# Kernel optimization log

Hardware: AMD Instinct MI355X
Metric: run time of the kernel (lower is better)

The kernel has to match this reference:

```python
import jax, jax.numpy as jnp
import numpy as np

B, S, D, H, DEPTH, VOCAB = 4096, 64, 512, 8, 4, 2
HD = D // H
EPS = 1e-5


def setup_inputs() -> dict:
    key = jax.random.key(0)
    ks = jax.random.split(key, 12)
    sc = 0.02
    return {
        "a_seq": jax.random.randint(ks[0], (B, S), 0, VOCAB, dtype=jnp.int32),
        "b_seq": jax.random.randint(ks[1], (B, S), 0, VOCAB, dtype=jnp.int32),
        "bit_emb": jax.random.normal(ks[2], (VOCAB, D), jnp.float32),
        "start_state": jax.random.normal(ks[3], (D,), jnp.float32),
        "ln1_g": jnp.ones((DEPTH, D), jnp.float32),
        "ln1_b": jnp.zeros((DEPTH, D), jnp.float32),
        # weights stored [in, out] (transpose of torch nn.Linear layout)
        "qkv_w": jax.random.normal(ks[4], (DEPTH, D, 3 * D), jnp.float32) * sc,
        "qkv_b": jnp.zeros((DEPTH, 3 * D), jnp.float32),
        "out_w": jax.random.normal(ks[5], (DEPTH, D, D), jnp.float32) * sc,
        "out_b": jnp.zeros((DEPTH, D), jnp.float32),
        "ln2_g": jnp.ones((DEPTH, D), jnp.float32),
        "ln2_b": jnp.zeros((DEPTH, D), jnp.float32),
        "ff1_w": jax.random.normal(ks[6], (DEPTH, D, 4 * D), jnp.float32) * sc,
        "ff1_b": jnp.zeros((DEPTH, 4 * D), jnp.float32),
        "ff2_w": jax.random.normal(ks[7], (DEPTH, 4 * D, D), jnp.float32) * sc,
        "ff2_b": jnp.zeros((DEPTH, D), jnp.float32),
        "head_w": jax.random.normal(ks[8], (D, 2), jnp.float32) * sc,
        "head_b": jnp.zeros((2,), jnp.float32),
    }


def _ln(x, g, b):
    m = x.mean(-1, keepdims=True)
    c = x - m
    v = (c * c).mean(-1, keepdims=True)
    return c * jax.lax.rsqrt(v + EPS) * g + b


def reference(a_seq, b_seq, bit_emb, start_state, ln1_g, ln1_b, qkv_w, qkv_b,
              out_w, out_b, ln2_g, ln2_b, ff1_w, ff1_b, ff2_w, ff2_b,
              head_w, head_b):
    # [B,S,D] combined bit embeddings, then time-major for scan
    emb = bit_emb[a_seq] + bit_emb[b_seq]
    xs = jnp.swapaxes(emb, 0, 1)  # [S,B,D]
    h0 = jnp.broadcast_to(start_state, (a_seq.shape[0], D))

    def step(h, xt):
        x = xt + h  # current_input = emb_a + emb_b + h_t, [B,D] (seq_len=1 squeezed)
        for l in range(DEPTH):  # pre-norm TransformerEncoderLayer, norm_first=True
            y = _ln(x, ln1_g[l], ln1_b[l])
            qkv = y @ qkv_w[l] + qkv_b[l]
            # self-attention over a single token: softmax of one score == 1,
            # so the attention output is exactly V (grads to Q,K are zero, as in torch)
            v = qkv[:, 2 * D:]
            x = x + v @ out_w[l] + out_b[l]
            y = _ln(x, ln2_g[l], ln2_b[l])
            x = x + jax.nn.relu(y @ ff1_w[l] + ff1_b[l]) @ ff2_w[l] + ff2_b[l]
        return x, x @ head_w + head_b

    _, logits = jax.lax.scan(step, h0, xs)  # [S,B,2]
    return jnp.swapaxes(logits, 0, 1)  # [B,S,2]
```

## Files before the change

### kernel.cpp

```cpp
#include <hip/hip_runtime.h>
#include <hip/hip_bf16.h>
#include <stdint.h>
#include <stddef.h>

#define B_ 4096
#define S_ 64
#define D_ 512
#define DEPTH_ 4


typedef __attribute__((ext_vector_type(8))) __bf16 bf16x8;
typedef __attribute__((ext_vector_type(4))) float f32x4;
typedef __hip_bfloat16 bf16_t;

__device__ __forceinline__ void async_copy16(const void* g, void* lds) {
  __builtin_amdgcn_global_load_lds(
      (const __attribute__((address_space(1))) void*)g,
      (__attribute__((address_space(3))) void*)lds, 16, 0, 0);
}

__device__ __forceinline__ float bf2f(bf16_t h) { return __bfloat162float(h); }

template<int TM, int TN, int EPI, int SPLITK>
__launch_bounds__(256)
__global__ void gemm_bf16(const bf16_t* __restrict__ A,
                          const bf16_t* __restrict__ Bt,
                          const float* __restrict__ bias,
                          bf16_t* __restrict__ O,
                          int M, int N, int K)
{
  constexpr int BK  = 64;
  constexpr int WM  = TM / 2, WN = TN / 2;
  constexpr int NMI = WM / 16, NNI = WN / 16;
  constexpr int CA  = TM / 8, CB = TN / 8;
  static_assert(TM * TN <= (TM + TN) * BK, "C tile must fit in staging LDS");

  __shared__ __align__(16) bf16_t smem[(TM + TN) * BK];
  bf16_t* sA = smem;
  bf16_t* sB = smem + TM * BK;

  const int tid  = threadIdx.x;
  const int lane = tid & 63;
  const int wave = tid >> 6;
  const int wm   = wave & 1;
  const int wn   = wave >> 1;
  const int m0   = blockIdx.x * TM;
  const int n0   = blockIdx.y * TN;
  const int KS   = K / SPLITK;
  const int kbeg = blockIdx.z * KS;

  const int lr = lane >> 3;
  const int lc = (lane & 7) * 8;

  f32x4 acc[NMI][NNI];
#pragma unroll
  for (int mi = 0; mi < NMI; ++mi)
#pragma unroll
    for (int ni = 0; ni < NNI; ++ni)
      acc[mi][ni] = (f32x4){0.f, 0.f, 0.f, 0.f};

  for (int k0 = kbeg; k0 < kbeg + KS; k0 += BK) {
#pragma unroll
    for (int c = wave; c < CA; c += 4) {
      const bf16_t* g = A + (size_t)(m0 + c * 8 + lr) * K + (k0 + lc);
      async_copy16(g, (char*)sA + c * 1024);
    }
#pragma unroll
    for (int c = wave; c < CB; c += 4) {
      const bf16_t* g = Bt + (size_t)(n0 + c * 8 + lr) * K + (k0 + lc);
      async_copy16(g, (char*)sB + c * 1024);
    }
    __syncthreads();

#pragma unroll
    for (int kk = 0; kk < BK; kk += 32) {
      bf16x8 af[NMI], bfv[NNI];
#pragma unroll
      for (int mi = 0; mi < NMI; ++mi)
        af[mi] = *(const bf16x8*)&sA[(wm * WM + mi * 16 + (lane & 15)) * BK + kk + (lane >> 4) * 8];
#pragma unroll
      for (int ni = 0; ni < NNI; ++ni)
        bfv[ni] = *(const bf16x8*)&sB[(wn * WN + ni * 16 + (lane & 15)) * BK + kk + (lane >> 4) * 8];
#pragma unroll
      for (int mi = 0; mi < NMI; ++mi)
#pragma unroll
        for (int ni = 0; ni < NNI; ++ni)
          acc[mi][ni] = __builtin_amdgcn_mfma_f32_16x16x32_bf16(af[mi], bfv[ni], acc[mi][ni], 0, 0, 0);
    }
    __syncthreads();
  }

  bf16_t* sC = smem;
#pragma unroll
  for (int mi = 0; mi < NMI; ++mi) {
#pragma unroll
    for (int ni = 0; ni < NNI; ++ni) {
      const int col  = wn * WN + ni * 16 + (lane & 15);
      const int row0 = wm * WM + mi * 16 + ((lane >> 4) << 2);
      const float bv = (SPLITK == 1 || blockIdx.z == 0) ? bias[n0 + col] : 0.f;
#pragma unroll
      for (int r = 0; r < 4; ++r) {
        float v = acc[mi][ni][r] + bv;
        if constexpr (EPI == 1) v = v > 0.f ? v : 0.f;
        sC[(row0 + r) * TN + col] = __float2bfloat16(v);
      }
    }
  }
  __syncthreads();
  bf16_t* Ob = O + (EPI == 2 ? (size_t)blockIdx.z * M * N : (size_t)0);
#pragma unroll
  for (int p = 0; p < (TM * TN) / 2048; ++p) {
    const int chunk = p * 256 + tid;
    const int rr = chunk / (TN / 8);
    const int cc = (chunk % (TN / 8)) * 8;
    *(uint4*)&Ob[(size_t)(m0 + rr) * N + n0 + cc] = *(const uint4*)&sC[rr * TN + cc];
  }
}

__device__ __forceinline__ void ln_store(const float v[8],
                                         const float* __restrict__ gamma,
                                         const float* __restrict__ beta,
                                         bf16_t* yrow, int lane)
{
  float s = 0.f, ss = 0.f;
#pragma unroll
  for (int i = 0; i < 8; ++i) { s += v[i]; ss += v[i] * v[i]; }
#pragma unroll
  for (int o = 32; o; o >>= 1) { s += __shfl_xor(s, o); ss += __shfl_xor(ss, o); }
  const float m   = s * (1.f / D_);
  const float inv = rsqrtf(ss * (1.f / D_) - m * m + 1e-5f);
  const int c0 = lane * 8;
  float g[8], b[8];
  *(float4*)&g[0] = *(const float4*)&gamma[c0];
  *(float4*)&g[4] = *(const float4*)&gamma[c0 + 4];
  *(float4*)&b[0] = *(const float4*)&beta[c0];
  *(float4*)&b[4] = *(const float4*)&beta[c0 + 4];
  alignas(16) bf16_t o8[8];
#pragma unroll
  for (int i = 0; i < 8; ++i)
    o8[i] = __float2bfloat16((v[i] - m) * inv * g[i] + b[i]);
  *(uint4*)&yrow[c0] = *(const uint4*)o8;
}

__device__ __forceinline__ void fold_p(float v[8], const bf16_t* pz)
{
  alignas(16) bf16_t t[8];
  *(uint4*)t = *(const uint4*)pz;
#pragma unroll
  for (int i = 0; i < 8; ++i) v[i] += bf2f(t[i]);
}

template<int NZ>
__global__ void ln_sumN_kernel(float* __restrict__ X,
                               const bf16_t* __restrict__ P,
                               const float* __restrict__ gamma,
                               const float* __restrict__ beta,
                               bf16_t* __restrict__ Y)
{
  const int row  = blockIdx.x * 4 + (threadIdx.x >> 6);
  const int lane = threadIdx.x & 63;
  const int c0 = lane * 8;
  float* xr = X + (size_t)row * D_;
  float v[8];
  *(float4*)&v[0] = *(const float4*)&xr[c0];
  *(float4*)&v[4] = *(const float4*)&xr[c0 + 4];
#pragma unroll
  for (int z = 0; z < NZ; ++z)
    fold_p(v, P + (size_t)z * B_ * D_ + (size_t)row * D_ + c0);
  *(float4*)&xr[c0]     = *(const float4*)&v[0];
  *(float4*)&xr[c0 + 4] = *(const float4*)&v[4];
  ln_store(v, gamma, beta, Y + (size_t)row * D_, lane);
}

__launch_bounds__(256)
__global__ void lnfold_gemm(const float* __restrict__ Xin,
                            const bf16_t* __restrict__ P,
                            float* __restrict__ Xout,
                            const float* __restrict__ gamma,
                            const float* __restrict__ beta,
                            const bf16_t* __restrict__ Bt,
                            const float* __restrict__ bias,
                            bf16_t* __restrict__ O)
{
  constexpr int TM = 32, TN = 128, BK = 64;
  __shared__ __align__(16) bf16_t sY[TM * D_];
  __shared__ __align__(16) bf16_t sB[TN * BK];

  const int tid  = threadIdx.x;
  const int lane = tid & 63;
  const int wave = tid >> 6;
  const int m0   = blockIdx.x * TM;
  const int n0   = blockIdx.y * TN;
  const int c0   = lane * 8;

#pragma unroll
  for (int i = 0; i < 8; ++i) {
    const int row  = wave * 8 + i;
    const int grow = m0 + row;
    const float* xr = Xin + (size_t)grow * D_ + c0;
    float v[8];
    *(float4*)&v[0] = *(const float4*)&xr[0];
    *(float4*)&v[4] = *(const float4*)&xr[4];
#pragma unroll
    for (int z = 0; z < 4; ++z)
      fold_p(v, P + (size_t)z * B_ * D_ + (size_t)grow * D_ + c0);
    if (blockIdx.y == 0) {
      float* xo = Xout + (size_t)grow * D_ + c0;
      *(float4*)&xo[0] = *(const float4*)&v[0];
      *(float4*)&xo[4] = *(const float4*)&v[4];
    }
    ln_store(v, gamma, beta, &sY[row * D_], lane);
  }

  f32x4 acc[2][2];
#pragma unroll
  for (int mi = 0; mi < 2; ++mi)
#pragma unroll
    for (int ni = 0; ni < 2; ++ni)
      acc[mi][ni] = (f32x4){0.f, 0.f, 0.f, 0.f};

  const int lr = lane >> 3;
  const int lc = (lane & 7) * 8;
  for (int k0 = 0; k0 < D_; k0 += BK) {
#pragma unroll
    for (int c = wave; c < TN / 8; c += 4) {
      const bf16_t* g = Bt + (size_t)(n0 + c * 8 + lr) * D_ + (k0 + lc);
      async_copy16(g, (char*)sB + c * 1024);
    }
    __syncthreads();
#pragma unroll
    for (int kk = 0; kk < BK; kk += 32) {
      bf16x8 af[2], bfv[2];
#pragma unroll
      for (int mi = 0; mi < 2; ++mi)
        af[mi] = *(const bf16x8*)&sY[(mi * 16 + (lane & 15)) * D_ + k0 + kk + (lane >> 4) * 8];
#pragma unroll
      for (int ni = 0; ni < 2; ++ni)
        bfv[ni] = *(const bf16x8*)&sB[(wave * 32 + ni * 16 + (lane & 15)) * BK + kk + (lane >> 4) * 8];
#pragma unroll
      for (int mi = 0; mi < 2; ++mi)
#pragma unroll
        for (int ni = 0; ni < 2; ++ni)
          acc[mi][ni] = __builtin_amdgcn_mfma_f32_16x16x32_bf16(af[mi], bfv[ni], acc[mi][ni], 0, 0, 0);
    }
    __syncthreads();
  }

  bf16_t* sC = sY;
#pragma unroll
  for (int mi = 0; mi < 2; ++mi) {
#pragma unroll
    for (int ni = 0; ni < 2; ++ni) {
      const int col  = wave * 32 + ni * 16 + (lane & 15);
      const int row0 = mi * 16 + ((lane >> 4) << 2);
      const float bv = bias[n0 + col];
#pragma unroll
      for (int r = 0; r < 4; ++r)
        sC[(row0 + r) * TN + col] = __float2bfloat16(acc[mi][ni][r] + bv);
    }
  }
  __syncthreads();
#pragma unroll
  for (int p = 0; p < (TM * TN) / 2048; ++p) {
    const int chunk = p * 256 + tid;
    const int rr = chunk / (TN / 8);
    const int cc = (chunk % (TN / 8)) * 8;
    *(uint4*)&O[(size_t)(m0 + rr) * D_ + n0 + cc] = *(const uint4*)&sC[rr * TN + cc];
  }
}

__global__ void add_ln_kernel(const int* __restrict__ a_seq,
                              const int* __restrict__ b_seq,
                              const float* __restrict__ bit_emb,
                              const float* __restrict__ hsrc, int hstride,
                              const bf16_t* __restrict__ P,
                              float* __restrict__ X,
                              const float* __restrict__ gamma,
                              const float* __restrict__ beta,
                              bf16_t* __restrict__ Y, int t,
                              const float* __restrict__ hw,
                              const float* __restrict__ hb,
                              float* __restrict__ out)
{
  const int row  = blockIdx.x * 4 + (threadIdx.x >> 6);
  const int lane = threadIdx.x & 63;
  const int ai = a_seq[row * S_ + t];
  const int bi = b_seq[row * S_ + t];
  const int c0 = lane * 8;
  float* xr = X + (size_t)row * D_;
  const float* pr = hsrc + (size_t)row * hstride + c0;
  float ea[8], eb[8], p[8], v[8];
  *(float4*)&ea[0] = *(const float4*)&bit_emb[ai * D_ + c0];
  *(float4*)&ea[4] = *(const float4*)&bit_emb[ai * D_ + c0 + 4];
  *(float4*)&eb[0] = *(const float4*)&bit_emb[bi * D_ + c0];
  *(float4*)&eb[4] = *(const float4*)&bit_emb[bi * D_ + c0 + 4];
  *(float4*)&p[0]  = *(const float4*)&pr[0];
  *(float4*)&p[4]  = *(const float4*)&pr[4];

  if (P != nullptr) {
#pragma unroll
    for (int z = 0; z < 4; ++z)
      fold_p(p, P + (size_t)z * B_ * D_ + (size_t)row * D_ + c0);
  }

  if (out != nullptr) {
    float w[16];
#pragma unroll
    for (int i = 0; i < 4; ++i)
      *(float4*)&w[i * 4] = *(const float4*)&hw[lane * 16 + i * 4];
    float s0 = 0.f, s1 = 0.f;
#pragma unroll
    for (int i = 0; i < 8; ++i) { s0 += p[i] * w[2 * i]; s1 += p[i] * w[2 * i + 1]; }
#pragma unroll
    for (int o = 32; o; o >>= 1) { s0 += __shfl_xor(s0, o); s1 += __shfl_xor(s1, o); }
    if (lane == 0) {
      float* po = out + (size_t)row * (S_ * 2) + (t - 1) * 2;
      po[0] = s0 + hb[0];
      po[1] = s1 + hb[1];
    }
  }

#pragma unroll
  for (int i = 0; i < 8; ++i) v[i] = ea[i] + eb[i] + p[i];
  *(float4*)&xr[c0]     = *(const float4*)&v[0];
  *(float4*)&xr[c0 + 4] = *(const float4*)&v[4];
  ln_store(v, gamma, beta, Y + (size_t)row * D_, lane);
}

__global__ void head_kernel(const float* __restrict__ X,
                            const bf16_t* __restrict__ P,
                            const float* __restrict__ hw,
                            const float* __restrict__ hb,
                            float* __restrict__ out, int t)
{
  const int row  = blockIdx.x * 4 + (threadIdx.x >> 6);
  const int lane = threadIdx.x & 63;
  const float* xr = X + (size_t)row * D_;
  const int c0 = lane * 8;
  float v[8];
  *(float4*)&v[0] = *(const float4*)&xr[c0];
  *(float4*)&v[4] = *(const float4*)&xr[c0 + 4];
#pragma unroll
  for (int z = 0; z < 4; ++z)
    fold_p(v, P + (size_t)z * B_ * D_ + (size_t)row * D_ + c0);
  float w[16];
#pragma unroll
  for (int i = 0; i < 4; ++i)
    *(float4*)&w[i * 4] = *(const float4*)&hw[lane * 16 + i * 4];
  float s0 = 0.f, s1 = 0.f;
#pragma unroll
  for (int i = 0; i < 8; ++i) { s0 += v[i] * w[2 * i]; s1 += v[i] * w[2 * i + 1]; }
#pragma unroll
  for (int o = 32; o; o >>= 1) { s0 += __shfl_xor(s0, o); s1 += __shfl_xor(s1, o); }
  if (lane == 0) {
    float* po = out + (size_t)row * (S_ * 2) + t * 2;
    po[0] = s0 + hb[0];
    po[1] = s1 + hb[1];
  }
}

__global__ void prep_wc(const float* __restrict__ qkv_w,
                        const float* __restrict__ out_w,
                        float* __restrict__ wc)
{
  const int n = blockIdx.x * 256 + threadIdx.x;
  const int k = blockIdx.y;
  const int l = blockIdx.z;
  const float* qrow = qkv_w + ((size_t)l * D_ + k) * (3 * D_) + 2 * D_;
  const float* ow   = out_w + (size_t)l * D_ * D_;
  float acc = 0.f;
  for (int j = 0; j < D_; ++j) acc += qrow[j] * ow[(size_t)j * D_ + n];
  wc[((size_t)l * D_ + k) * D_ + n] = acc;
}

__global__ void prep_bc(const float* __restrict__ qkv_b,
                        const float* __restrict__ out_w,
                        const float* __restrict__ out_b,
                        float* __restrict__ bc)
{
  const int l = blockIdx.x;
  const int n = threadIdx.x;
  const float* qb = qkv_b + (size_t)l * (3 * D_) + 2 * D_;
  const float* ow = out_w + (size_t)l * D_ * D_;
  float acc = out_b[(size_t)l * D_ + n];
  for (int j = 0; j < D_; ++j) acc += qb[j] * ow[(size_t)j * D_ + n];
  bc[(size_t)l * D_ + n] = acc;
}

__global__ void transpose_conv(const float* __restrict__ src,
                               bf16_t* __restrict__ dst, int R, int C)
{
  __shared__ float tile[32][33];
  const int l = blockIdx.z;
  const float* s = src + (size_t)l * R * C;
  bf16_t* d = dst + (size_t)l * R * C;
  const int c0 = blockIdx.x * 32, r0 = blockIdx.y * 32;
  const int tx = threadIdx.x, ty = threadIdx.y;
  tile[ty][tx] = s[(size_t)(r0 + ty) * C + (c0 + tx)];
  __syncthreads();
  d[(size_t)(c0 + ty) * R + (r0 + tx)] = __float2bfloat16(tile[tx][ty]);
}

extern "C" void kernel_launch(void* const* d_in, const int* in_sizes, int n_in,
                              void* d_out, int out_size, void* d_ws, size_t ws_size,
                              hipStream_t stream)
{
  const int*   a_seq     = (const int*)  d_in[0];
  const int*   b_seq     = (const int*)  d_in[1];
  const float* bit_emb   = (const float*)d_in[2];
  const float* start     = (const float*)d_in[3];
  const float* ln1_g     = (const float*)d_in[4];
  const float* ln1_b     = (const float*)d_in[5];
  const float* qkv_w     = (const float*)d_in[6];
  const float* qkv_b     = (const float*)d_in[7];
  const float* out_w     = (const float*)d_in[8];
  const float* out_b     = (const float*)d_in[9];
  const float* ln2_g     = (const float*)d_in[10];
  const float* ln2_b     = (const float*)d_in[11];
  const float* ff1_w     = (const float*)d_in[12];
  const float* ff1_b     = (const float*)d_in[13];
  const float* ff2_w     = (const float*)d_in[14];
  const float* ff2_b     = (const float*)d_in[15];
  const float* head_w    = (const float*)d_in[16];
  const float* head_b    = (const float*)d_in[17];
  float* out = (float*)d_out;

  char* ws = (char*)d_ws;
  float*  XA    = (float*) ws; ws += (size_t)B_ * D_ * 4;
  bf16_t* Y     = (bf16_t*)ws; ws += (size_t)B_ * D_ * 2;
  bf16_t* U     = (bf16_t*)ws; ws += (size_t)B_ * 4 * D_ * 2;
  bf16_t* WCT   = (bf16_t*)ws; ws += (size_t)DEPTH_ * D_ * D_ * 2;
  bf16_t* FF1T  = (bf16_t*)ws; ws += (size_t)DEPTH_ * D_ * 4 * D_ * 2;
  bf16_t* FF2T  = (bf16_t*)ws; ws += (size_t)DEPTH_ * 4 * D_ * D_ * 2;
  float*  BC    = (float*) ws; ws += (size_t)DEPTH_ * D_ * 4;
  float*  WCTMP = (float*) ws; ws += (size_t)DEPTH_ * D_ * D_ * 4;
  bf16_t* PSPL  = (bf16_t*)ws; ws += (size_t)4 * B_ * D_ * 2;
  bf16_t* P1    = (bf16_t*)ws; ws += (size_t)B_ * D_ * 2;
  float*  XB    = (float*) ws; ws += (size_t)B_ * D_ * 4;

  prep_wc<<<dim3(2, 512, 4), 256, 0, stream>>>(qkv_w, out_w, WCTMP);
  prep_bc<<<4, 512, 0, stream>>>(qkv_b, out_w, out_b, BC);
  transpose_conv<<<dim3(16, 16, 4),  dim3(32, 32), 0, stream>>>(WCTMP, WCT, 512, 512);
  transpose_conv<<<dim3(64, 16, 4),  dim3(32, 32), 0, stream>>>(ff1_w, FF1T, 512, 2048);
  transpose_conv<<<dim3(16, 64, 4),  dim3(32, 32), 0, stream>>>(ff2_w, FF2T, 2048, 512);

  for (int t = 0; t < S_; ++t) {
    if (t == 0)
      add_ln_kernel<<<B_ / 4, 256, 0, stream>>>(a_seq, b_seq, bit_emb, start, 0,
                                                nullptr, XA, ln1_g, ln1_b, Y, t,
                                                head_w, head_b, nullptr);
    else
      add_ln_kernel<<<B_ / 4, 256, 0, stream>>>(a_seq, b_seq, bit_emb, XB, D_,
                                                PSPL, XA, ln1_g, ln1_b, Y, t,
                                                head_w, head_b, out);
    for (int l = 0; l < DEPTH_; ++l) {
      float* Xcur;
      if (l == 0) {
        gemm_bf16<64, 64, 2, 1><<<dim3(64, 8), 256, 0, stream>>>(
            Y, WCT, BC, P1, B_, D_, D_);
        Xcur = XA;
      } else {
        float* Xin  = (l & 1) ? XA : XB;
        float* Xout = (l & 1) ? XB : XA;
        lnfold_gemm<<<dim3(B_ / 32, 4), 256, 0, stream>>>(
            Xin, PSPL, Xout,
            ln1_g + (size_t)l * D_, ln1_b + (size_t)l * D_,
            WCT + (size_t)l * D_ * D_, BC + (size_t)l * D_, P1);
        Xcur = Xout;
      }
      ln_sumN_kernel<1><<<B_ / 4, 256, 0, stream>>>(Xcur, P1,
                                                    ln2_g + (size_t)l * D_,
                                                    ln2_b + (size_t)l * D_, Y);
      gemm_bf16<128, 128, 1, 1><<<dim3(32, 16), 256, 0, stream>>>(
          Y, FF1T + (size_t)l * D_ * 4 * D_, ff1_b + (size_t)l * 4 * D_, U,
          B_, 4 * D_, D_);
      gemm_bf16<128, 128, 2, 4><<<dim3(32, 4, 4), 256, 0, stream>>>(
          U, FF2T + (size_t)l * 4 * D_ * D_, ff2_b + (size_t)l * D_, PSPL,
          B_, D_, 4 * D_);
    }
  }
  head_kernel<<<B_ / 4, 256, 0, stream>>>(XB, PSPL, head_w, head_b, out, S_ - 1);
}
```

Before: 14.91 ms.

## Fuse add+LN into QKV GEMM and LN2 into FF1 GEMM, halve FF2 split-K

Replaces the standalone add/LN kernel and the first-layer projection GEMM with a single addln_gemm kernel. Replaces the ln_sumN plus FF1 GEMM pair with ff1_fused, which folds the residual, applies LN2 into LDS and runs the FF1 GEMM with ReLU in one kernel. The FF2 split-K drops from 4 to 2 with a 128x64 tile, so fewer partial buffers have to be folded downstream. Residual buffers now ping-pong between XA and XB. This removes the bf16 Y round trips and several launches per layer. In exchange, each N-block recomputes the LayerNorm, and the small 32-row M tile means the weights are reused less per block.

```diff
diff --git a/kernel.cpp b/kernel.cpp
--- a/kernel.cpp
+++ b/kernel.cpp
@@ -13,6 +13,8 @@
 typedef __attribute__((ext_vector_type(4))) float f32x4;
 typedef __hip_bfloat16 bf16_t;
 
+constexpr int SPLITZ = 2;
+
 __device__ __forceinline__ void async_copy16(const void* g, void* lds) {
   __builtin_amdgcn_global_load_lds(
       (const __attribute__((address_space(1))) void*)g,
@@ -21,100 +23,12 @@
 
 __device__ __forceinline__ float bf2f(bf16_t h) { return __bfloat162float(h); }
 
-template<int TM, int TN, int EPI, int SPLITK>
-__launch_bounds__(256)
-__global__ void gemm_bf16(const bf16_t* __restrict__ A,
-                          const bf16_t* __restrict__ Bt,
-                          const float* __restrict__ bias,
-                          bf16_t* __restrict__ O,
-                          int M, int N, int K)
-{
-  constexpr int BK  = 64;
-  constexpr int WM  = TM / 2, WN = TN / 2;
-  constexpr int NMI = WM / 16, NNI = WN / 16;
-  constexpr int CA  = TM / 8, CB = TN / 8;
-  static_assert(TM * TN <= (TM + TN) * BK, "C tile must fit in staging LDS");
-
-  __shared__ __align__(16) bf16_t smem[(TM + TN) * BK];
-  bf16_t* sA = smem;
-  bf16_t* sB = smem + TM * BK;
-
-  const int tid  = threadIdx.x;
-  const int lane = tid & 63;
-  const int wave = tid >> 6;
-  const int wm   = wave & 1;
-  const int wn   = wave >> 1;
-  const int m0   = blockIdx.x * TM;
-  const int n0   = blockIdx.y * TN;
-  const int KS   = K / SPLITK;
-  const int kbeg = blockIdx.z * KS;
-
-  const int lr = lane >> 3;
-  const int lc = (lane & 7) * 8;
-
-  f32x4 acc[NMI][NNI];
-#pragma unroll
-  for (int mi = 0; mi < NMI; ++mi)
-#pragma unroll
-    for (int ni = 0; ni < NNI; ++ni)
-      acc[mi][ni] = (f32x4){0.f, 0.f, 0.f, 0.f};
-
-  for (int k0 = kbeg; k0 < kbeg + KS; k0 += BK) {
-#pragma unroll
-    for (int c = wave; c < CA; c += 4) {
-      const bf16_t* g = A + (size_t)(m0 + c * 8 + lr) * K + (k0 + lc);
-      async_copy16(g, (char*)sA + c * 1024);
-    }
-#pragma unroll
-    for (int c = wave; c < CB; c += 4) {
-      const bf16_t* g = Bt + (size_t)(n0 + c * 8 + lr) * K + (k0 + lc);
-      async_copy16(g, (char*)sB + c * 1024);
-    }
-    __syncthreads();
-
-#pragma unroll
-    for (int kk = 0; kk < BK; kk += 32) {
-      bf16x8 af[NMI], bfv[NNI];
-#pragma unroll
-      for (int mi = 0; mi < NMI; ++mi)
-        af[mi] = *(const bf16x8*)&sA[(wm * WM + mi * 16 + (lane & 15)) * BK + kk + (lane >> 4) * 8];
-#pragma unroll
-      for (int ni = 0; ni < NNI; ++ni)
-        bfv[ni] = *(const bf16x8*)&sB[(wn * WN + ni * 16 + (lane & 15)) * BK + kk + (lane >> 4) * 8];
-#pragma unroll
-      for (int mi = 0; mi < NMI; ++mi)
-#pragma unroll
-        for (int ni = 0; ni < NNI; ++ni)
-          acc[mi][ni] = __builtin_amdgcn_mfma_f32_16x16x32_bf16(af[mi], bfv[ni], acc[mi][ni], 0, 0, 0);
-    }
-    __syncthreads();
-  }
-
-  bf16_t* sC = smem;
-#pragma unroll
-  for (int mi = 0; mi < NMI; ++mi) {
-#pragma unroll
-    for (int ni = 0; ni < NNI; ++ni) {
-      const int col  = wn * WN + ni * 16 + (lane & 15);
-      const int row0 = wm * WM + mi * 16 + ((lane >> 4) << 2);
-      const float bv = (SPLITK == 1 || blockIdx.z == 0) ? bias[n0 + col] : 0.f;
-#pragma unroll
-      for (int r = 0; r < 4; ++r) {
-        float v = acc[mi][ni][r] + bv;
-        if constexpr (EPI == 1) v = v > 0.f ? v : 0.f;
-        sC[(row0 + r) * TN + col] = __float2bfloat16(v);
-      }
-    }
-  }
-  __syncthreads();
-  bf16_t* Ob = O + (EPI == 2 ? (size_t)blockIdx.z * M * N : (size_t)0);
-#pragma unroll
-  for (int p = 0; p < (TM * TN) / 2048; ++p) {
-    const int chunk = p * 256 + tid;
-    const int rr = chunk / (TN / 8);
-    const int cc = (chunk % (TN / 8)) * 8;
-    *(uint4*)&Ob[(size_t)(m0 + rr) * N + n0 + cc] = *(const uint4*)&sC[rr * TN + cc];
-  }
+__device__ __forceinline__ void fold_p(float v[8], const bf16_t* pz)
+{
+  alignas(16) bf16_t t[8];
+  *(uint4*)t = *(const uint4*)pz;
+#pragma unroll
+  for (int i = 0; i < 8; ++i) v[i] += bf2f(t[i]);
 }
 
 __device__ __forceinline__ void ln_store(const float v[8],
@@ -142,34 +56,100 @@
   *(uint4*)&yrow[c0] = *(const uint4*)o8;
 }
 
-__device__ __forceinline__ void fold_p(float v[8], const bf16_t* pz)
-{
-  alignas(16) bf16_t t[8];
-  *(uint4*)t = *(const uint4*)pz;
-#pragma unroll
-  for (int i = 0; i < 8; ++i) v[i] += bf2f(t[i]);
-}
-
-template<int NZ>
-__global__ void ln_sumN_kernel(float* __restrict__ X,
-                               const bf16_t* __restrict__ P,
-                               const float* __restrict__ gamma,
-                               const float* __restrict__ beta,
-                               bf16_t* __restrict__ Y)
-{
-  const int row  = blockIdx.x * 4 + (threadIdx.x >> 6);
-  const int lane = threadIdx.x & 63;
-  const int c0 = lane * 8;
-  float* xr = X + (size_t)row * D_;
-  float v[8];
-  *(float4*)&v[0] = *(const float4*)&xr[c0];
-  *(float4*)&v[4] = *(const float4*)&xr[c0 + 4];
-#pragma unroll
-  for (int z = 0; z < NZ; ++z)
-    fold_p(v, P + (size_t)z * B_ * D_ + (size_t)row * D_ + c0);
-  *(float4*)&xr[c0]     = *(const float4*)&v[0];
-  *(float4*)&xr[c0 + 4] = *(const float4*)&v[4];
-  ln_store(v, gamma, beta, Y + (size_t)row * D_, lane);
+template<int TM, int TN, int EPI, int SPLITK>
+__launch_bounds__(256)
+__global__ void gemm_bf16(const bf16_t* __restrict__ A,
+                          const bf16_t* __restrict__ Bt,
+                          const float* __restrict__ bias,
+                          bf16_t* __restrict__ O,
+                          int M, int N, int K)
+{
+  constexpr int BK  = 64;
+  constexpr int WM  = TM / 2, WN = TN / 2;
+  constexpr int NMI = WM / 16, NNI = WN / 16;
+  constexpr int CA  = TM / 8, CB = TN / 8;
+  static_assert(TM * TN <= (TM + TN) * BK, "C tile must fit in staging LDS");
+
+  __shared__ __align__(16) bf16_t smem[(TM + TN) * BK];
+  bf16_t* sA = smem;
+  bf16_t* sB = smem + TM * BK;
+
+  const int tid  = threadIdx.x;
+  const int lane = tid & 63;
+  const int wave = tid >> 6;
+  const int wm   = wave & 1;
+  const int wn   = wave >> 1;
+  const int m0   = blockIdx.x * TM;
+  const int n0   = blockIdx.y * TN;
+  const int KS   = K / SPLITK;
+  const int kbeg = blockIdx.z * KS;
+
+  const int lr = lane >> 3;
+  const int lc = (lane & 7) * 8;
+
+  f32x4 acc[NMI][NNI];
+#pragma unroll
+  for (int mi = 0; mi < NMI; ++mi)
+#pragma unroll
+    for (int ni = 0; ni < NNI; ++ni)
+      acc[mi][ni] = (f32x4){0.f, 0.f, 0.f, 0.f};
+
+  for (int k0 = kbeg; k0 < kbeg + KS; k0 += BK) {
+#pragma unroll
+    for (int c = wave; c < CA; c += 4) {
+      const bf16_t* g = A + (size_t)(m0 + c * 8 + lr) * K + (k0 + lc);
+      async_copy16(g, (char*)sA + c * 1024);
+    }
+#pragma unroll
+    for (int c = wave; c < CB; c += 4) {
+      const bf16_t* g = Bt + (size_t)(n0 + c * 8 + lr) * K + (k0 + lc);
+      async_copy16(g, (char*)sB + c * 1024);
+    }
+    __syncthreads();
+
+#pragma unroll
+    for (int kk = 0; kk < BK; kk += 32) {
+      bf16x8 af[NMI], bfv[NNI];
+#pragma unroll
+      for (int mi = 0; mi < NMI; ++mi)
+        af[mi] = *(const bf16x8*)&sA[(wm * WM + mi * 16 + (lane & 15)) * BK + kk + (lane >> 4) * 8];
+#pragma unroll
+      for (int ni = 0; ni < NNI; ++ni)
+        bfv[ni] = *(const bf16x8*)&sB[(wn * WN + ni * 16 + (lane & 15)) * BK + kk + (lane >> 4) * 8];
+#pragma unroll
+      for (int mi = 0; mi < NMI; ++mi)
+#pragma unroll
+        for (int ni = 0; ni < NNI; ++ni)
+          acc[mi][ni] = __builtin_amdgcn_mfma_f32_16x16x32_bf16(af[mi], bfv[ni], acc[mi][ni], 0, 0, 0);
+    }
+    __syncthreads();
+  }
+
+  bf16_t* sC = smem;
+#pragma unroll
+  for (int mi = 0; mi < NMI; ++mi) {
+#pragma unroll
+    for (int ni = 0; ni < NNI; ++ni) {
+      const int col  = wn * WN + ni * 16 + (lane & 15);
+      const int row0 = wm * WM + mi * 16 + ((lane >> 4) << 2);
+      const float bv = (SPLITK == 1 || blockIdx.z == 0) ? bias[n0 + col] : 0.f;
+#pragma unroll
+      for (int r = 0; r < 4; ++r) {
+        float v = acc[mi][ni][r] + bv;
+        if constexpr (EPI == 1) v = v > 0.f ? v : 0.f;
+        sC[(row0 + r) * TN + col] = __float2bfloat16(v);
+      }
+    }
+  }
+  __syncthreads();
+  bf16_t* Ob = O + (EPI == 2 ? (size_t)blockIdx.z * M * N : (size_t)0);
+#pragma unroll
+  for (int p = 0; p < (TM * TN) / 2048; ++p) {
+    const int chunk = p * 256 + tid;
+    const int rr = chunk / (TN / 8);
+    const int cc = (chunk % (TN / 8)) * 8;
+    *(uint4*)&Ob[(size_t)(m0 + rr) * N + n0 + cc] = *(const uint4*)&sC[rr * TN + cc];
+  }
 }
 
 __launch_bounds__(256)
@@ -202,7 +182,7 @@
     *(float4*)&v[0] = *(const float4*)&xr[0];
     *(float4*)&v[4] = *(const float4*)&xr[4];
 #pragma unroll
-    for (int z = 0; z < 4; ++z)
+    for (int z = 0; z < SPLITZ; ++z)
       fold_p(v, P + (size_t)z * B_ * D_ + (size_t)grow * D_ + c0);
     if (blockIdx.y == 0) {
       float* xo = Xout + (size_t)grow * D_ + c0;
@@ -269,62 +249,236 @@
   }
 }
 
-__global__ void add_ln_kernel(const int* __restrict__ a_seq,
-                              const int* __restrict__ b_seq,
-                              const float* __restrict__ bit_emb,
-                              const float* __restrict__ hsrc, int hstride,
-                              const bf16_t* __restrict__ P,
-                              float* __restrict__ X,
-                              const float* __restrict__ gamma,
-                              const float* __restrict__ beta,
-                              bf16_t* __restrict__ Y, int t,
-                              const float* __restrict__ hw,
-                              const float* __restrict__ hb,
-                              float* __restrict__ out)
-{
-  const int row  = blockIdx.x * 4 + (threadIdx.x >> 6);
-  const int lane = threadIdx.x & 63;
-  const int ai = a_seq[row * S_ + t];
-  const int bi = b_seq[row * S_ + t];
-  const int c0 = lane * 8;
-  float* xr = X + (size_t)row * D_;
-  const float* pr = hsrc + (size_t)row * hstride + c0;
-  float ea[8], eb[8], p[8], v[8];
-  *(float4*)&ea[0] = *(const float4*)&bit_emb[ai * D_ + c0];
-  *(float4*)&ea[4] = *(const float4*)&bit_emb[ai * D_ + c0 + 4];
-  *(float4*)&eb[0] = *(const float4*)&bit_emb[bi * D_ + c0];
-  *(float4*)&eb[4] = *(const float4*)&bit_emb[bi * D_ + c0 + 4];
-  *(float4*)&p[0]  = *(const float4*)&pr[0];
-  *(float4*)&p[4]  = *(const float4*)&pr[4];
-
-  if (P != nullptr) {
-#pragma unroll
-    for (int z = 0; z < 4; ++z)
-      fold_p(p, P + (size_t)z * B_ * D_ + (size_t)row * D_ + c0);
-  }
-
-  if (out != nullptr) {
-    float w[16];
+__launch_bounds__(256)
+__global__ void addln_gemm(const int* __restrict__ a_seq,
+                           const int* __restrict__ b_seq,
+                           const float* __restrict__ bit_emb,
+                           const float* __restrict__ hsrc, int hstride,
+                           const bf16_t* __restrict__ P,
+                           float* __restrict__ Xout,
+                           const float* __restrict__ gamma,
+                           const float* __restrict__ beta,
+                           const bf16_t* __restrict__ Bt,
+                           const float* __restrict__ bias,
+                           bf16_t* __restrict__ O,
+                           int t,
+                           const float* __restrict__ hw,
+                           const float* __restrict__ hb,
+                           float* __restrict__ out)
+{
+  constexpr int TM = 32, TN = 128, BK = 64;
+  __shared__ __align__(16) bf16_t sY[TM * D_];
+  __shared__ __align__(16) bf16_t sB[TN * BK];
+
+  const int tid  = threadIdx.x;
+  const int lane = tid & 63;
+  const int wave = tid >> 6;
+  const int m0   = blockIdx.x * TM;
+  const int n0   = blockIdx.y * TN;
+  const int c0   = lane * 8;
+
+  const bool do_head = (out != nullptr) && (blockIdx.y == 0);
+  float w[16];
+  if (do_head) {
 #pragma unroll
     for (int i = 0; i < 4; ++i)
       *(float4*)&w[i * 4] = *(const float4*)&hw[lane * 16 + i * 4];
-    float s0 = 0.f, s1 = 0.f;
-#pragma unroll
-    for (int i = 0; i < 8; ++i) { s0 += p[i] * w[2 * i]; s1 += p[i] * w[2 * i + 1]; }
-#pragma unroll
-    for (int o = 32; o; o >>= 1) { s0 += __shfl_xor(s0, o); s1 += __shfl_xor(s1, o); }
-    if (lane == 0) {
-      float* po = out + (size_t)row * (S_ * 2) + (t - 1) * 2;
-      po[0] = s0 + hb[0];
-      po[1] = s1 + hb[1];
-    }
-  }
-
-#pragma unroll
-  for (int i = 0; i < 8; ++i) v[i] = ea[i] + eb[i] + p[i];
-  *(float4*)&xr[c0]     = *(const float4*)&v[0];
-  *(float4*)&xr[c0 + 4] = *(const float4*)&v[4];
-  ln_store(v, gamma, beta, Y + (size_t)row * D_, lane);
+  }
+
+#pragma unroll
+  for (int i = 0; i < 8; ++i) {
+    const int row  = wave * 8 + i;
+    const int grow = m0 + row;
+    const int ai = a_seq[grow * S_ + t];
+    const int bi = b_seq[grow * S_ + t];
+    const float* pr = hsrc + (size_t)grow * hstride + c0;
+    float p[8];
+    *(float4*)&p[0] = *(const float4*)&pr[0];
+    *(float4*)&p[4] = *(const float4*)&pr[4];
+    if (P != nullptr) {
+#pragma unroll
+      for (int z = 0; z < SPLITZ; ++z)
+        fold_p(p, P + (size_t)z * B_ * D_ + (size_t)grow * D_ + c0);
+    }
+    if (do_head) {
+      float s0 = 0.f, s1 = 0.f;
+#pragma unroll
+      for (int j = 0; j < 8; ++j) { s0 += p[j] * w[2 * j]; s1 += p[j] * w[2 * j + 1]; }
+#pragma unroll
+      for (int o = 32; o; o >>= 1) { s0 += __shfl_xor(s0, o); s1 += __shfl_xor(s1, o); }
+      if (lane == 0) {
+        float* po = out + (size_t)grow * (S_ * 2) + (t - 1) * 2;
+        po[0] = s0 + hb[0];
+        po[1] = s1 + hb[1];
+      }
+    }
+    float ea[8], eb[8], v[8];
+    *(float4*)&ea[0] = *(const float4*)&bit_emb[ai * D_ + c0];
+    *(float4*)&ea[4] = *(const float4*)&bit_emb[ai * D_ + c0 + 4];
+    *(float4*)&eb[0] = *(const float4*)&bit_emb[bi * D_ + c0];
+    *(float4*)&eb[4] = *(const float4*)&bit_emb[bi * D_ + c0 + 4];
+#pragma unroll
+    for (int j = 0; j < 8; ++j) v[j] = ea[j] + eb[j] + p[j];
+    if (blockIdx.y == 0) {
+      float* xo = Xout + (size_t)grow * D_ + c0;
+      *(float4*)&xo[0] = *(const float4*)&v[0];
+      *(float4*)&xo[4] = *(const float4*)&v[4];
+    }
+    ln_store(v, gamma, beta, &sY[row * D_], lane);
+  }
+
+  f32x4 acc[2][2];
+#pragma unroll
+  for (int mi = 0; mi < 2; ++mi)
+#pragma unroll
+    for (int ni = 0; ni < 2; ++ni)
+      acc[mi][ni] = (f32x4){0.f, 0.f, 0.f, 0.f};
+
+  const int lr = lane >> 3;
+  const int lc = (lane & 7) * 8;
+  for (int k0 = 0; k0 < D_; k0 += BK) {
+#pragma unroll
+    for (int c = wave; c < TN / 8; c += 4) {
+      const bf16_t* g = Bt + (size_t)(n0 + c * 8 + lr) * D_ + (k0 + lc);
+      async_copy16(g, (char*)sB + c * 1024);
+    }
+    __syncthreads();
+#pragma unroll
+    for (int kk = 0; kk < BK; kk += 32) {
+      bf16x8 af[2], bfv[2];
+#pragma unroll
+      for (int mi = 0; mi < 2; ++mi)
+        af[mi] = *(const bf16x8*)&sY[(mi * 16 + (lane & 15)) * D_ + k0 + kk + (lane >> 4) * 8];
+#pragma unroll
+      for (int ni = 0; ni < 2; ++ni)
+        bfv[ni] = *(const bf16x8*)&sB[(wave * 32 + ni * 16 + (lane & 15)) * BK + kk + (lane >> 4) * 8];
+#pragma unroll
+      for (int mi = 0; mi < 2; ++mi)
+#pragma unroll
+        for (int ni = 0; ni < 2; ++ni)
+          acc[mi][ni] = __builtin_amdgcn_mfma_f32_16x16x32_bf16(af[mi], bfv[ni], acc[mi][ni], 0, 0, 0);
+    }
+    __syncthreads();
+  }
+
+  bf16_t* sC = sY;
+#pragma unroll
+  for (int mi = 0; mi < 2; ++mi) {
+#pragma unroll
+    for (int ni = 0; ni < 2; ++ni) {
+      const int col  = wave * 32 + ni * 16 + (lane & 15);
+      const int row0 = mi * 16 + ((lane >> 4) << 2);
+      const float bv = bias[n0 + col];
+#pragma unroll
+      for (int r = 0; r < 4; ++r)
+        sC[(row0 + r) * TN + col] = __float2bfloat16(acc[mi][ni][r] + bv);
+    }
+  }
+  __syncthreads();
+#pragma unroll
+  for (int p = 0; p < (TM * TN) / 2048; ++p) {
+    const int chunk = p * 256 + tid;
+    const int rr = chunk / (TN / 8);
+    const int cc = (chunk % (TN / 8)) * 8;
+    *(uint4*)&O[(size_t)(m0 + rr) * D_ + n0 + cc] = *(const uint4*)&sC[rr * TN + cc];
+  }
+}
+
+__launch_bounds__(256)
+__global__ void ff1_fused(const float* __restrict__ Xin,
+                          const bf16_t* __restrict__ P1,
+                          float* __restrict__ Xout,
+                          const float* __restrict__ gamma,
+                          const float* __restrict__ beta,
+                          const bf16_t* __restrict__ Bt,
+                          const float* __restrict__ bias,
+                          bf16_t* __restrict__ U)
+{
+  constexpr int TM = 32, TN = 256, BK = 64, NFF = 4 * D_;
+  __shared__ __align__(16) bf16_t sY[TM * D_];
+  __shared__ __align__(16) bf16_t sB[TN * BK];
+
+  const int tid  = threadIdx.x;
+  const int lane = tid & 63;
+  const int wave = tid >> 6;
+  const int m0   = blockIdx.x * TM;
+  const int n0   = blockIdx.y * TN;
+  const int c0   = lane * 8;
+
+#pragma unroll
+  for (int i = 0; i < 8; ++i) {
+    const int row  = wave * 8 + i;
+    const int grow = m0 + row;
+    const float* xr = Xin + (size_t)grow * D_ + c0;
+    float v[8];
+    *(float4*)&v[0] = *(const float4*)&xr[0];
+    *(float4*)&v[4] = *(const float4*)&xr[4];
+    fold_p(v, P1 + (size_t)grow * D_ + c0);
+    if (blockIdx.y == 0) {
+      float* xo = Xout + (size_t)grow * D_ + c0;
+      *(float4*)&xo[0] = *(const float4*)&v[0];
+      *(float4*)&xo[4] = *(const float4*)&v[4];
+    }
+    ln_store(v, gamma, beta, &sY[row * D_], lane);
+  }
+
+  f32x4 acc[2][4];
+#pragma unroll
+  for (int mi = 0; mi < 2; ++mi)
+#pragma unroll
+    for (int ni = 0; ni < 4; ++ni)
+      acc[mi][ni] = (f32x4){0.f, 0.f, 0.f, 0.f};
+
+  const int lr = lane >> 3;
+  const int lc = (lane & 7) * 8;
+  for (int k0 = 0; k0 < D_; k0 += BK) {
+#pragma unroll
+    for (int c = wave; c < TN / 8; c += 4) {
+      const bf16_t* g = Bt + (size_t)(n0 + c * 8 + lr) * D_ + (k0 + lc);
+      async_copy16(g, (char*)sB + c * 1024);
+    }
+    __syncthreads();
+#pragma unroll
+    for (int kk = 0; kk < BK; kk += 32) {
+      bf16x8 af[2], bfv[4];
+#pragma unroll
+      for (int mi = 0; mi < 2; ++mi)
+        af[mi] = *(const bf16x8*)&sY[(mi * 16 + (lane & 15)) * D_ + k0 + kk + (lane >> 4) * 8];
+#pragma unroll
+      for (int ni = 0; ni < 4; ++ni)
+        bfv[ni] = *(const bf16x8*)&sB[(wave * 64 + ni * 16 + (lane & 15)) * BK + kk + (lane >> 4) * 8];
+#pragma unroll
+      for (int mi = 0; mi < 2; ++mi)
+#pragma unroll
+        for (int ni = 0; ni < 4; ++ni)
+          acc[mi][ni] = __builtin_amdgcn_mfma_f32_16x16x32_bf16(af[mi], bfv[ni], acc[mi][ni], 0, 0, 0);
+    }
+    __syncthreads();
+  }
+
+  bf16_t* sC = sY;
+#pragma unroll
+  for (int mi = 0; mi < 2; ++mi) {
+#pragma unroll
+    for (int ni = 0; ni < 4; ++ni) {
+      const int col  = wave * 64 + ni * 16 + (lane & 15);
+      const int row0 = mi * 16 + ((lane >> 4) << 2);
+      const float bv = bias[n0 + col];
+#pragma unroll
+      for (int r = 0; r < 4; ++r) {
+        float v = acc[mi][ni][r] + bv;
+        sC[(row0 + r) * TN + col] = __float2bfloat16(v > 0.f ? v : 0.f);
+      }
+    }
+  }
+  __syncthreads();
+#pragma unroll
+  for (int p = 0; p < (TM * TN) / 2048; ++p) {
+    const int chunk = p * 256 + tid;
+    const int rr = chunk >> 5;
+    const int cc = (chunk & 31) * 8;
+    *(uint4*)&U[(size_t)(m0 + rr) * NFF + n0 + cc] = *(const uint4*)&sC[rr * TN + cc];
+  }
 }
 
 __global__ void head_kernel(const float* __restrict__ X,
@@ -341,7 +495,7 @@
   *(float4*)&v[0] = *(const float4*)&xr[c0];
   *(float4*)&v[4] = *(const float4*)&xr[c0 + 4];
 #pragma unroll
-  for (int z = 0; z < 4; ++z)
+  for (int z = 0; z < SPLITZ; ++z)
     fold_p(v, P + (size_t)z * B_ * D_ + (size_t)row * D_ + c0);
   float w[16];
 #pragma unroll
@@ -427,16 +581,15 @@
 
   char* ws = (char*)d_ws;
   float*  XA    = (float*) ws; ws += (size_t)B_ * D_ * 4;
-  bf16_t* Y     = (bf16_t*)ws; ws += (size_t)B_ * D_ * 2;
+  float*  XB    = (float*) ws; ws += (size_t)B_ * D_ * 4;
   bf16_t* U     = (bf16_t*)ws; ws += (size_t)B_ * 4 * D_ * 2;
   bf16_t* WCT   = (bf16_t*)ws; ws += (size_t)DEPTH_ * D_ * D_ * 2;
   bf16_t* FF1T  = (bf16_t*)ws; ws += (size_t)DEPTH_ * D_ * 4 * D_ * 2;
   bf16_t* FF2T  = (bf16_t*)ws; ws += (size_t)DEPTH_ * 4 * D_ * D_ * 2;
   float*  BC    = (float*) ws; ws += (size_t)DEPTH_ * D_ * 4;
   float*  WCTMP = (float*) ws; ws += (size_t)DEPTH_ * D_ * D_ * 4;
-  bf16_t* PSPL  = (bf16_t*)ws; ws += (size_t)4 * B_ * D_ * 2;
+  bf16_t* PSPL  = (bf16_t*)ws; ws += (size_t)SPLITZ * B_ * D_ * 2;
   bf16_t* P1    = (bf16_t*)ws; ws += (size_t)B_ * D_ * 2;
-  float*  XB    = (float*) ws; ws += (size_t)B_ * D_ * 4;
 
   prep_wc<<<dim3(2, 512, 4), 256, 0, stream>>>(qkv_w, out_w, WCTMP);
   prep_bc<<<4, 512, 0, stream>>>(qkv_b, out_w, out_b, BC);
@@ -446,35 +599,29 @@
 
   for (int t = 0; t < S_; ++t) {
     if (t == 0)
-      add_ln_kernel<<<B_ / 4, 256, 0, stream>>>(a_seq, b_seq, bit_emb, start, 0,
-                                                nullptr, XA, ln1_g, ln1_b, Y, t,
-                                                head_w, head_b, nullptr);
+      addln_gemm<<<dim3(B_ / 32, 4), 256, 0, stream>>>(
+          a_seq, b_seq, bit_emb, start, 0, nullptr, XA,
+          ln1_g, ln1_b, WCT, BC, P1, t, head_w, head_b, nullptr);
     else
-      add_ln_kernel<<<B_ / 4, 256, 0, stream>>>(a_seq, b_seq, bit_emb, XB, D_,
-                                                PSPL, XA, ln1_g, ln1_b, Y, t,
-                                                head_w, head_b, out);
+      addln_gemm<<<dim3(B_ / 32, 4), 256, 0, stream>>>(
+          a_seq, b_seq, bit_emb, XB, D_, PSPL, XA,
+          ln1_g, ln1_b, WCT, BC, P1, t, head_w, head_b, out);
+    float* cur = XA;
+    float* alt = XB;
     for (int l = 0; l < DEPTH_; ++l) {
-      float* Xcur;
-      if (l == 0) {
-        gemm_bf16<64, 64, 2, 1><<<dim3(64, 8), 256, 0, stream>>>(
-            Y, WCT, BC, P1, B_, D_, D_);
-        Xcur = XA;
-      } else {
-        float* Xin  = (l & 1) ? XA : XB;
-        float* Xout = (l & 1) ? XB : XA;
+      if (l > 0) {
         lnfold_gemm<<<dim3(B_ / 32, 4), 256, 0, stream>>>(
-            Xin, PSPL, Xout,
+            cur, PSPL, alt,
             ln1_g + (size_t)l * D_, ln1_b + (size_t)l * D_,
             WCT + (size_t)l * D_ * D_, BC + (size_t)l * D_, P1);
-        Xcur = Xout;
+        float* tmp = cur; cur = alt; alt = tmp;
       }
-      ln_sumN_kernel<1><<<B_ / 4, 256, 0, stream>>>(Xcur, P1,
-                                                    ln2_g + (size_t)l * D_,
-                                                    ln2_b + (size_t)l * D_, Y);
-      gemm_bf16<128, 128, 1, 1><<<dim3(32, 16), 256, 0, stream>>>(
-          Y, FF1T + (size_t)l * D_ * 4 * D_, ff1_b + (size_t)l * 4 * D_, U,
-          B_, 4 * D_, D_);
-      gemm_bf16<128, 128, 2, 4><<<dim3(32, 4, 4), 256, 0, stream>>>(
+      ff1_fused<<<dim3(B_ / 32, 8), 256, 0, stream>>>(
+          cur, P1, alt,
+          ln2_g + (size_t)l * D_, ln2_b + (size_t)l * D_,
+          FF1T + (size_t)l * D_ * 4 * D_, ff1_b + (size_t)l * 4 * D_, U);
+      { float* tmp = cur; cur = alt; alt = tmp; }
+      gemm_bf16<128, 64, 2, SPLITZ><<<dim3(32, 8, SPLITZ), 256, 0, stream>>>(
           U, FF2T + (size_t)l * 4 * D_ * D_, ff2_b + (size_t)l * D_, PSPL,
           B_, D_, 4 * D_);
     }
```

Result: slower. 18.43 ms (+23.7%).
